# Optimization experiments

Hardware: AMD Instinct MI355X
Metric: run time of the kernel (lower is better)

The kernel has to match this reference:

```python
import jax, jax.numpy as jnp
import numpy as np

GRID = 64            # volume_pixel per axis
VOX = 1.0 / GRID     # voxel_physical (unit-cube volume_physical)
CHUNK = 128          # gaussians per scan step


def _voxel_centers():
    # [V,3] centers of voxels of a unit cube, V = GRID**3
    c = (jnp.arange(GRID, dtype=jnp.float32) + 0.5) * VOX
    zz, yy, xx = jnp.meshgrid(c, c, c, indexing='ij')
    return jnp.stack([xx.ravel(), yy.ravel(), zz.ravel()], axis=-1)


def _quat_to_rotmat(q):
    # q: [N,4] (w,x,y,z), normalized -> [N,3,3]
    q = q / jnp.linalg.norm(q, axis=-1, keepdims=True)
    w, x, y, z = q[:, 0], q[:, 1], q[:, 2], q[:, 3]
    return jnp.stack([
        jnp.stack([1 - 2 * (y * y + z * z), 2 * (x * y - w * z), 2 * (x * z + w * y)], -1),
        jnp.stack([2 * (x * y + w * z), 1 - 2 * (x * x + z * z), 2 * (y * z - w * x)], -1),
        jnp.stack([2 * (x * z - w * y), 2 * (y * z + w * x), 1 - 2 * (x * x + y * y)], -1),
    ], axis=-2)


def _voxelize(means3D, densities, scales, rotations):
    N = means3D.shape[0]
    R = _quat_to_rotmat(rotations)                       # [N,3,3]
    inv_s2 = 1.0 / (scales * scales)                     # [N,3]
    # Sigma^{-1} = R diag(1/s^2) R^T
    Sinv = jnp.einsum('nij,nj,nkj->nik', R, inv_s2, R)   # [N,3,3]
    centers = _voxel_centers()                            # [V,3]
    n_chunks = N // CHUNK
    mu_c = means3D.reshape(n_chunks, CHUNK, 3)
    de_c = densities.reshape(n_chunks, CHUNK)
    Si_c = Sinv.reshape(n_chunks, CHUNK, 3, 3)

    def step(vol, xs):
        mu, dens, Si = xs
        d = centers[None, :, :] - mu[:, None, :]                 # [C,V,3]
        qf = jnp.einsum('cvi,cij,cvj->cv', d, Si, d)             # [C,V]
        vol = vol + jnp.sum(dens[:, None] * jnp.exp(-0.5 * qf), axis=0)
        return vol, None

    vol0 = jnp.zeros((GRID ** 3,), dtype=means3D.dtype)
    volume, _ = jax.lax.scan(step, vol0, (mu_c, de_c, Si_c))
    volume = volume.reshape(GRID, GRID, GRID)
    # screen-space-style radius: 3 sigma of the largest axis, in voxels
    radii = jnp.ceil(3.0 * jnp.max(scales, axis=-1) / VOX).astype(jnp.int32)
    return volume, radii


def setup_inputs() -> dict:
    key = jax.random.key(0)
    k1, k2, k3, k4 = jax.random.split(key, 4)
    N = 4096
    means3D = jax.random.uniform(k1, (N, 3), dtype=jnp.float32)                 # in unit cube
    densities = jax.random.uniform(k2, (N,), dtype=jnp.float32)
    scales = jax.random.uniform(k3, (N, 3), dtype=jnp.float32) * 0.05 + 0.01    # 0.6-3.8 voxels
    rotations = jax.random.normal(k4, (N, 4), dtype=jnp.float32)
    return {"means3D": means3D, "densities": densities, "scales": scales, "rotations": rotations}


def reference(means3D, densities, scales, rotations):
    return _voxelize(means3D, densities, scales, rotations)
```

## Files before the change

kernel.cpp:

```cpp
#include <hip/hip_runtime.h>

#define GRIDN 64
#define NVOX (GRIDN * GRIDN * GRIDN)
#define VOXF (1.0f / 64.0f)
#define QCUT 16.0f
#define EXPSCL (-0.72134752044f)
#define SKIPTH (QCUT * EXPSCL)

#define WS_CULLA 0
#define WS_CULLB (4 * 4096)
#define WS_REC   (8 * 4096)

__global__ __launch_bounds__(256) void prep_kernel(
    const float* __restrict__ means, const float* __restrict__ dens,
    const float* __restrict__ scales, const float* __restrict__ rots,
    float* __restrict__ ws, float* __restrict__ radii_out, int N)
{
    int i = blockIdx.x * 256 + threadIdx.x;
    if (i >= N) return;

    float qw = rots[i * 4 + 0], qx = rots[i * 4 + 1];
    float qy = rots[i * 4 + 2], qz = rots[i * 4 + 3];
    float inm = rsqrtf(qw * qw + qx * qx + qy * qy + qz * qz);
    qw *= inm; qx *= inm; qy *= inm; qz *= inm;
    float r00 = 1.f - 2.f * (qy * qy + qz * qz);
    float r01 = 2.f * (qx * qy - qw * qz);
    float r02 = 2.f * (qx * qz + qw * qy);
    float r10 = 2.f * (qx * qy + qw * qz);
    float r11 = 1.f - 2.f * (qx * qx + qz * qz);
    float r12 = 2.f * (qy * qz - qw * qx);
    float r20 = 2.f * (qx * qz - qw * qy);
    float r21 = 2.f * (qy * qz + qw * qx);
    float r22 = 1.f - 2.f * (qx * qx + qy * qy);

    float s0 = scales[i * 3 + 0], s1 = scales[i * 3 + 1], s2 = scales[i * 3 + 2];
    float v0 = s0 * s0, v1 = s1 * s1, v2 = s2 * s2;
    float i0 = 1.f / v0, i1 = 1.f / v1, i2 = 1.f / v2;

    float A = (r00 * r00 * i0 + r01 * r01 * i1 + r02 * r02 * i2) * EXPSCL;
    float B = (r10 * r10 * i0 + r11 * r11 * i1 + r12 * r12 * i2) * EXPSCL;
    float C = (r20 * r20 * i0 + r21 * r21 * i1 + r22 * r22 * i2) * EXPSCL;
    float D = (r00 * r10 * i0 + r01 * r11 * i1 + r02 * r12 * i2) * EXPSCL;
    float E = (r00 * r20 * i0 + r01 * r21 * i1 + r02 * r22 * i2) * EXPSCL;
    float F = (r10 * r20 * i0 + r11 * r21 * i1 + r12 * r22 * i2) * EXPSCL;

    float Cxx = r00 * r00 * v0 + r01 * r01 * v1 + r02 * r02 * v2;
    float Cyy = r10 * r10 * v0 + r11 * r11 * v1 + r12 * r12 * v2;
    float Czz = r20 * r20 * v0 + r21 * r21 * v1 + r22 * r22 * v2;

    float de = fmaxf(dens[i], 1e-30f);
    float qeff = fmaxf(QCUT + 2.0f * logf(de), 0.0f);
    float smax2 = fmaxf(v0, fmaxf(v1, v2));

    float mx = means[i * 3 + 0], my = means[i * 3 + 1], mz = means[i * 3 + 2];
    float4 ca; ca.x = mx; ca.y = my; ca.z = mz; ca.w = sqrtf(qeff * Cxx);
    float4 cb; cb.x = sqrtf(qeff * Cyy); cb.y = sqrtf(qeff * Czz);
    cb.z = qeff * smax2; cb.w = 0.f;
    ((float4*)(ws + WS_CULLA))[i] = ca;
    ((float4*)(ws + WS_CULLB))[i] = cb;

    float4* R = (float4*)(ws + WS_REC + (size_t)i * 16);
    float4 w0; w0.x = A; w0.y = B; w0.z = C; w0.w = 2.f * D;
    float4 w1; w1.x = 2.f * E; w1.y = 2.f * F; w1.z = -0.25f / A; w1.w = log2f(de);
    float4 w2; w2.x = mx; w2.y = my; w2.z = mz; w2.w = 0.f;
    R[0] = w0; R[1] = w1; R[2] = w2;

    float m = fmaxf(s0, fmaxf(s1, s2));
    radii_out[i] = ceilf(m * 3.0f * 64.0f);

    if (i == 0) {
        float4 z; z.x = 0.f; z.y = 0.f; z.z = 0.f; z.w = 0.f;
        float4 d1; d1.x = 0.f; d1.y = 0.f; d1.z = 0.f; d1.w = -1e30f;
        float4* Dm = (float4*)(ws + WS_REC + (size_t)N * 16);
        Dm[0] = z; Dm[1] = d1; Dm[2] = z;
    }
}

#define BODY(v0_, v1_, v2_) do {                                              \
    float dy = py - v2_.y, dz = pz - v2_.z;                                   \
    float tt  = fmaf(v1_.y, dy, v0_.z * dz);                                  \
    float qyz = fmaf(v0_.y * dy, dy, fmaf(tt, dz, v1_.w));                    \
    float gx  = fmaf(v0_.w, dy, v1_.x * dz);                                  \
    float qmx = fmaf(gx * gx, v1_.z, qyz);                                    \
    if (!__all(qmx < SKIPTH)) {                                               \
        float dx0 = px - v2_.x;                                               \
        float dx1 = dx0 + VOXF, dx2 = dx0 + 2.f * VOXF, dx3 = dx0 + 3.f * VOXF;\
        acc.x += __builtin_amdgcn_exp2f(fmaf(dx0, fmaf(v0_.x, dx0, gx), qyz));\
        acc.y += __builtin_amdgcn_exp2f(fmaf(dx1, fmaf(v0_.x, dx1, gx), qyz));\
        acc.z += __builtin_amdgcn_exp2f(fmaf(dx2, fmaf(v0_.x, dx2, gx), qyz));\
        acc.w += __builtin_amdgcn_exp2f(fmaf(dx3, fmaf(v0_.x, dx3, gx), qyz));\
    }                                                                         \
} while (0)

__global__ __launch_bounds__(512, 8) void vox_kernel(
    const float* __restrict__ ws, float* __restrict__ out, int N)
{
    __shared__ unsigned long long cmask[64];
    __shared__ int slist[4096];
    __shared__ float4 plds[8][64];

    const float* rec = ws + WS_REC;
    const int tid = threadIdx.x;
    const int lane = tid & 63, wave = tid >> 6;
    const int t = (blockIdx.x * 421) & 1023;
    const int tX = t & 7, tY = (t >> 3) & 7, tZ = t >> 6;
    const int x = (tX << 3) + ((lane & 1) << 2);
    const int y = (tY << 3) + ((lane >> 1) & 7);
    const int z = (tZ << 2) + (lane >> 4);
    const float px = (x + 0.5f) * VOXF;
    const float py = (y + 0.5f) * VOXF;
    const float pz = (z + 0.5f) * VOXF;

    const float lox = ((tX << 3) + 0.5f) * VOXF, hix = ((tX << 3) + 7.5f) * VOXF;
    const float loy = ((tY << 3) + 0.5f) * VOXF, hiy = ((tY << 3) + 7.5f) * VOXF;
    const float loz = ((tZ << 2) + 0.5f) * VOXF, hiz = ((tZ << 2) + 3.5f) * VOXF;

    const int nch = (N + 63) >> 6;
    #pragma unroll
    for (int k = 0; k < 8; ++k) {
        const int c = (wave << 3) + k;
        unsigned long long bal = 0ull;
        if (c < nch) {
            const int gi = (c << 6) + lane;
            const int gc = gi < N ? gi : N - 1;
            float4 ca = ((const float4*)(ws + WS_CULLA))[gc];
            float4 cb = ((const float4*)(ws + WS_CULLB))[gc];
            float cx = fminf(fmaxf(ca.x, lox), hix) - ca.x;
            float cy = fminf(fmaxf(ca.y, loy), hiy) - ca.y;
            float cz = fminf(fmaxf(ca.z, loz), hiz) - ca.z;
            float d2 = fmaf(cx, cx, fmaf(cy, cy, cz * cz));
            bool keep = (gi < N) && (d2 <= cb.z)
                && (ca.x + ca.w >= lox) && (ca.x - ca.w <= hix)
                && (ca.y + cb.x >= loy) && (ca.y - cb.x <= hiy)
                && (ca.z + cb.y >= loz) && (ca.z - cb.y <= hiz);
            bal = __ballot(keep);
        }
        if (lane == 0) cmask[(wave << 3) + k] = bal;
    }
    __syncthreads();

    unsigned long long mk = cmask[lane];
    int pc = __popcll(mk);
    int incl = pc;
    #pragma unroll
    for (int d = 1; d < 64; d <<= 1) {
        int t2 = __shfl_up(incl, d, 64);
        if (lane >= d) incl += t2;
    }
    const int excl = incl - pc;
    const int cnt = __builtin_amdgcn_readlane(incl, 63);

    #pragma unroll
    for (int k = 0; k < 8; ++k) {
        const int c = (wave << 3) + k;
        unsigned long long mc = cmask[c];
        int bse = __builtin_amdgcn_readlane(excl, c);
        if ((mc >> lane) & 1ull) {
            int pre = __popcll(mc & ((1ull << lane) - 1ull));
            slist[bse + pre] = (c << 6) + lane;
        }
    }

    const int L = ((cnt + 31) >> 5) << 2;
    const int padend = L << 3;
    for (int i = cnt + tid; i < padend; i += 512) slist[i] = N;
    __syncthreads();

    const int beg = wave * L, end = beg + L;
    float4 acc; acc.x = 0.f; acc.y = 0.f; acc.z = 0.f; acc.w = 0.f;

    for (int base = beg; base < end; base += 64) {
        int src = base + lane;
        int vidx = slist[src < padend ? src : padend - 1];
        int m = end - base; if (m > 64) m = 64;
        for (int j = 0; j < m; j += 4) {
            int i0 = __builtin_amdgcn_readlane(vidx, j);
            int i1 = __builtin_amdgcn_readlane(vidx, j + 1);
            int i2 = __builtin_amdgcn_readlane(vidx, j + 2);
            int i3 = __builtin_amdgcn_readlane(vidx, j + 3);
            const float4* P0 = (const float4*)(rec + ((size_t)i0 << 4));
            const float4* P1 = (const float4*)(rec + ((size_t)i1 << 4));
            const float4* P2 = (const float4*)(rec + ((size_t)i2 << 4));
            const float4* P3 = (const float4*)(rec + ((size_t)i3 << 4));
            float4 a0 = P0[0], a1 = P0[1], a2 = P0[2];
            float4 b0 = P1[0], b1 = P1[1], b2 = P1[2];
            float4 c0 = P2[0], c1 = P2[1], c2 = P2[2];
            float4 d0 = P3[0], d1 = P3[1], d2 = P3[2];
            BODY(a0, a1, a2);
            BODY(b0, b1, b2);
            BODY(c0, c1, c2);
            BODY(d0, d1, d2);
        }
    }

    plds[wave][lane] = acc;
    __syncthreads();

    if (wave == 0) {
        float4 r = plds[0][lane];
        #pragma unroll
        for (int w = 1; w < 8; ++w) {
            float4 p = plds[w][lane];
            r.x += p.x; r.y += p.y; r.z += p.z; r.w += p.w;
        }
        const int v = (z << 12) + (y << 6) + x;
        *(float4*)&out[v] = r;
    }
}

extern "C" void kernel_launch(void* const* d_in, const int* in_sizes, int n_in,
                              void* d_out, int out_size, void* d_ws, size_t ws_size,
                              hipStream_t stream)
{
    const float* means  = (const float*)d_in[0];
    const float* dens   = (const float*)d_in[1];
    const float* scales = (const float*)d_in[2];
    const float* rots   = (const float*)d_in[3];
    float* out = (float*)d_out;
    float* ws  = (float*)d_ws;
    const int N = in_sizes[1];

    prep_kernel<<<(N + 255) / 256, 256, 0, stream>>>(means, dens, scales, rots,
                                                     ws, out + NVOX, N);
    vox_kernel<<<1024, 512, 0, stream>>>(ws, out, N);
}
```

Before: 29.87 us.

## Add coarse-cell culling pass so voxel tiles scan only per-cell candidate lists

The prep kernel gains 128 extra blocks. Each one culls all gaussians against a coarse 16x16x8 cell, recomputing the bounds inline, and writes a compacted candidate index list plus a count to workspace. Each vox tile then reads only its parent cell's list instead of culling all N gaussians, and maps the list entries back to global indices. This cuts per-tile culling loads and compute, at the cost of a hierarchical two-level cull, redundant bound recomputation, and an extra indirection.

```diff
diff --git a/kernel.cpp b/kernel.cpp
--- a/kernel.cpp
+++ b/kernel.cpp
@@ -10,70 +10,144 @@
 #define WS_CULLA 0
 #define WS_CULLB (4 * 4096)
 #define WS_REC   (8 * 4096)
+#define WS_CLIST (28 * 4096)
+#define WS_CCNT  (28 * 4096 + 128 * 4096)
 
 __global__ __launch_bounds__(256) void prep_kernel(
     const float* __restrict__ means, const float* __restrict__ dens,
     const float* __restrict__ scales, const float* __restrict__ rots,
-    float* __restrict__ ws, float* __restrict__ radii_out, int N)
+    float* __restrict__ ws, int* __restrict__ clist, int* __restrict__ ccnt,
+    float* __restrict__ radii_out, int N)
 {
-    int i = blockIdx.x * 256 + threadIdx.x;
-    if (i >= N) return;
-
-    float qw = rots[i * 4 + 0], qx = rots[i * 4 + 1];
-    float qy = rots[i * 4 + 2], qz = rots[i * 4 + 3];
-    float inm = rsqrtf(qw * qw + qx * qx + qy * qy + qz * qz);
-    qw *= inm; qx *= inm; qy *= inm; qz *= inm;
-    float r00 = 1.f - 2.f * (qy * qy + qz * qz);
-    float r01 = 2.f * (qx * qy - qw * qz);
-    float r02 = 2.f * (qx * qz + qw * qy);
-    float r10 = 2.f * (qx * qy + qw * qz);
-    float r11 = 1.f - 2.f * (qx * qx + qz * qz);
-    float r12 = 2.f * (qy * qz - qw * qx);
-    float r20 = 2.f * (qx * qz - qw * qy);
-    float r21 = 2.f * (qy * qz + qw * qx);
-    float r22 = 1.f - 2.f * (qx * qx + qy * qy);
-
-    float s0 = scales[i * 3 + 0], s1 = scales[i * 3 + 1], s2 = scales[i * 3 + 2];
-    float v0 = s0 * s0, v1 = s1 * s1, v2 = s2 * s2;
-    float i0 = 1.f / v0, i1 = 1.f / v1, i2 = 1.f / v2;
-
-    float A = (r00 * r00 * i0 + r01 * r01 * i1 + r02 * r02 * i2) * EXPSCL;
-    float B = (r10 * r10 * i0 + r11 * r11 * i1 + r12 * r12 * i2) * EXPSCL;
-    float C = (r20 * r20 * i0 + r21 * r21 * i1 + r22 * r22 * i2) * EXPSCL;
-    float D = (r00 * r10 * i0 + r01 * r11 * i1 + r02 * r12 * i2) * EXPSCL;
-    float E = (r00 * r20 * i0 + r01 * r21 * i1 + r02 * r22 * i2) * EXPSCL;
-    float F = (r10 * r20 * i0 + r11 * r21 * i1 + r12 * r22 * i2) * EXPSCL;
-
-    float Cxx = r00 * r00 * v0 + r01 * r01 * v1 + r02 * r02 * v2;
-    float Cyy = r10 * r10 * v0 + r11 * r11 * v1 + r12 * r12 * v2;
-    float Czz = r20 * r20 * v0 + r21 * r21 * v1 + r22 * r22 * v2;
-
-    float de = fmaxf(dens[i], 1e-30f);
-    float qeff = fmaxf(QCUT + 2.0f * logf(de), 0.0f);
-    float smax2 = fmaxf(v0, fmaxf(v1, v2));
-
-    float mx = means[i * 3 + 0], my = means[i * 3 + 1], mz = means[i * 3 + 2];
-    float4 ca; ca.x = mx; ca.y = my; ca.z = mz; ca.w = sqrtf(qeff * Cxx);
-    float4 cb; cb.x = sqrtf(qeff * Cyy); cb.y = sqrtf(qeff * Czz);
-    cb.z = qeff * smax2; cb.w = 0.f;
-    ((float4*)(ws + WS_CULLA))[i] = ca;
-    ((float4*)(ws + WS_CULLB))[i] = cb;
-
-    float4* R = (float4*)(ws + WS_REC + (size_t)i * 16);
-    float4 w0; w0.x = A; w0.y = B; w0.z = C; w0.w = 2.f * D;
-    float4 w1; w1.x = 2.f * E; w1.y = 2.f * F; w1.z = -0.25f / A; w1.w = log2f(de);
-    float4 w2; w2.x = mx; w2.y = my; w2.z = mz; w2.w = 0.f;
-    R[0] = w0; R[1] = w1; R[2] = w2;
-
-    float m = fmaxf(s0, fmaxf(s1, s2));
-    radii_out[i] = ceilf(m * 3.0f * 64.0f);
-
-    if (i == 0) {
-        float4 z; z.x = 0.f; z.y = 0.f; z.z = 0.f; z.w = 0.f;
-        float4 d1; d1.x = 0.f; d1.y = 0.f; d1.z = 0.f; d1.w = -1e30f;
-        float4* Dm = (float4*)(ws + WS_REC + (size_t)N * 16);
-        Dm[0] = z; Dm[1] = d1; Dm[2] = z;
-    }
+    __shared__ int swseg[4][1024];
+    __shared__ int lenw[4];
+
+    const int nrec = (N + 255) >> 8;
+    const int b = blockIdx.x;
+
+    if (b < nrec) {
+        int i = b * 256 + threadIdx.x;
+        if (i >= N) return;
+
+        float qw = rots[i * 4 + 0], qx = rots[i * 4 + 1];
+        float qy = rots[i * 4 + 2], qz = rots[i * 4 + 3];
+        float inm = rsqrtf(qw * qw + qx * qx + qy * qy + qz * qz);
+        qw *= inm; qx *= inm; qy *= inm; qz *= inm;
+        float r00 = 1.f - 2.f * (qy * qy + qz * qz);
+        float r01 = 2.f * (qx * qy - qw * qz);
+        float r02 = 2.f * (qx * qz + qw * qy);
+        float r10 = 2.f * (qx * qy + qw * qz);
+        float r11 = 1.f - 2.f * (qx * qx + qz * qz);
+        float r12 = 2.f * (qy * qz - qw * qx);
+        float r20 = 2.f * (qx * qz - qw * qy);
+        float r21 = 2.f * (qy * qz + qw * qx);
+        float r22 = 1.f - 2.f * (qx * qx + qy * qy);
+
+        float s0 = scales[i * 3 + 0], s1 = scales[i * 3 + 1], s2 = scales[i * 3 + 2];
+        float v0 = s0 * s0, v1 = s1 * s1, v2 = s2 * s2;
+        float i0 = 1.f / v0, i1 = 1.f / v1, i2 = 1.f / v2;
+
+        float A = (r00 * r00 * i0 + r01 * r01 * i1 + r02 * r02 * i2) * EXPSCL;
+        float B = (r10 * r10 * i0 + r11 * r11 * i1 + r12 * r12 * i2) * EXPSCL;
+        float C = (r20 * r20 * i0 + r21 * r21 * i1 + r22 * r22 * i2) * EXPSCL;
+        float D = (r00 * r10 * i0 + r01 * r11 * i1 + r02 * r12 * i2) * EXPSCL;
+        float E = (r00 * r20 * i0 + r01 * r21 * i1 + r02 * r22 * i2) * EXPSCL;
+        float F = (r10 * r20 * i0 + r11 * r21 * i1 + r12 * r22 * i2) * EXPSCL;
+
+        float Cxx = r00 * r00 * v0 + r01 * r01 * v1 + r02 * r02 * v2;
+        float Cyy = r10 * r10 * v0 + r11 * r11 * v1 + r12 * r12 * v2;
+        float Czz = r20 * r20 * v0 + r21 * r21 * v1 + r22 * r22 * v2;
+
+        float de = fmaxf(dens[i], 1e-30f);
+        float qeff = fmaxf(QCUT + 2.0f * logf(de), 0.0f);
+        float smax2 = fmaxf(v0, fmaxf(v1, v2));
+
+        float mx = means[i * 3 + 0], my = means[i * 3 + 1], mz = means[i * 3 + 2];
+        float4 ca; ca.x = mx; ca.y = my; ca.z = mz; ca.w = sqrtf(qeff * Cxx);
+        float4 cb; cb.x = sqrtf(qeff * Cyy); cb.y = sqrtf(qeff * Czz);
+        cb.z = qeff * smax2; cb.w = 0.f;
+        ((float4*)(ws + WS_CULLA))[i] = ca;
+        ((float4*)(ws + WS_CULLB))[i] = cb;
+
+        float4* R = (float4*)(ws + WS_REC + (size_t)i * 16);
+        float4 w0; w0.x = A; w0.y = B; w0.z = C; w0.w = 2.f * D;
+        float4 w1; w1.x = 2.f * E; w1.y = 2.f * F; w1.z = -0.25f / A; w1.w = log2f(de);
+        float4 w2; w2.x = mx; w2.y = my; w2.z = mz; w2.w = 0.f;
+        R[0] = w0; R[1] = w1; R[2] = w2;
+
+        float m = fmaxf(s0, fmaxf(s1, s2));
+        radii_out[i] = ceilf(m * 3.0f * 64.0f);
+
+        if (i == 0) {
+            float4 zv; zv.x = 0.f; zv.y = 0.f; zv.z = 0.f; zv.w = 0.f;
+            float4 d1; d1.x = 0.f; d1.y = 0.f; d1.z = 0.f; d1.w = -1e30f;
+            float4* Dm = (float4*)(ws + WS_REC + (size_t)N * 16);
+            Dm[0] = zv; Dm[1] = d1; Dm[2] = zv;
+        }
+        return;
+    }
+
+    const int tid = threadIdx.x, lane = tid & 63, wave = tid >> 6;
+    const int cell = b - nrec;
+    const int cX = cell & 3, cY = (cell >> 2) & 3, cZ = cell >> 4;
+    const float lox = ((cX << 4) + 0.5f) * VOXF, hix = ((cX << 4) + 15.5f) * VOXF;
+    const float loy = ((cY << 4) + 0.5f) * VOXF, hiy = ((cY << 4) + 15.5f) * VOXF;
+    const float loz = ((cZ << 3) + 0.5f) * VOXF, hiz = ((cZ << 3) + 7.5f) * VOXF;
+
+    const int nch = (N + 63) >> 6;
+    int off = 0;
+    for (int j = 0; j < 16; ++j) {
+        const int c = (wave << 4) + j;
+        if (c >= nch) break;
+        const int gi = (c << 6) + lane;
+        const int gc = gi < N ? gi : N - 1;
+
+        float qw = rots[gc * 4 + 0], qx = rots[gc * 4 + 1];
+        float qy = rots[gc * 4 + 2], qz = rots[gc * 4 + 3];
+        float r00, r10, r20, r01, r11, r21, r02, r12, r22;
+        {
+            float inm = rsqrtf(qw * qw + qx * qx + qy * qy + qz * qz);
+            float w = qw * inm, a = qx * inm, bq = qy * inm, cq = qz * inm;
+            r00 = 1.f - 2.f * (bq * bq + cq * cq); r01 = 2.f * (a * bq - w * cq);
+            r02 = 2.f * (a * cq + w * bq);         r10 = 2.f * (a * bq + w * cq);
+            r11 = 1.f - 2.f * (a * a + cq * cq);   r12 = 2.f * (bq * cq - w * a);
+            r20 = 2.f * (a * cq - w * bq);         r21 = 2.f * (bq * cq + w * a);
+            r22 = 1.f - 2.f * (a * a + bq * bq);
+        }
+        float s0 = scales[gc * 3 + 0], s1 = scales[gc * 3 + 1], s2 = scales[gc * 3 + 2];
+        float v0 = s0 * s0, v1 = s1 * s1, v2 = s2 * s2;
+        float Cxx = r00 * r00 * v0 + r01 * r01 * v1 + r02 * r02 * v2;
+        float Cyy = r10 * r10 * v0 + r11 * r11 * v1 + r12 * r12 * v2;
+        float Czz = r20 * r20 * v0 + r21 * r21 * v1 + r22 * r22 * v2;
+        float de = fmaxf(dens[gc], 1e-30f);
+        float qeff = fmaxf(QCUT + 2.0f * logf(de), 0.0f);
+        float rx = sqrtf(qeff * Cxx), ry = sqrtf(qeff * Cyy), rz = sqrtf(qeff * Czz);
+        float sph = qeff * fmaxf(v0, fmaxf(v1, v2));
+        float mx = means[gc * 3 + 0], my = means[gc * 3 + 1], mz = means[gc * 3 + 2];
+
+        float cx = fminf(fmaxf(mx, lox), hix) - mx;
+        float cy = fminf(fmaxf(my, loy), hiy) - my;
+        float cz = fminf(fmaxf(mz, loz), hiz) - mz;
+        float d2 = fmaf(cx, cx, fmaf(cy, cy, cz * cz));
+        bool keep = (gi < N) && (d2 <= sph)
+            && (mx + rx >= lox) && (mx - rx <= hix)
+            && (my + ry >= loy) && (my - ry <= hiy)
+            && (mz + rz >= loz) && (mz - rz <= hiz);
+
+        unsigned long long bal = __ballot(keep);
+        int pre = __popcll(bal & ((1ull << lane) - 1ull));
+        if (keep) swseg[wave][off + pre] = gi;
+        off += __popcll(bal);
+    }
+    if (lane == 0) lenw[wave] = off;
+    __syncthreads();
+
+    const int l0 = lenw[0], l1 = lenw[1], l2 = lenw[2];
+    const int mybase = (wave > 0 ? l0 : 0) + (wave > 1 ? l1 : 0) + (wave > 2 ? l2 : 0);
+    const int mylen = lenw[wave];
+    int* dst = clist + (size_t)cell * 4096;
+    for (int i = lane; i < mylen; i += 64) dst[mybase + i] = swseg[wave][i];
+    if (tid == 0) ccnt[cell] = l0 + l1 + l2 + lenw[3];
 }
 
 #define BODY(v0_, v1_, v2_) do {                                              \
@@ -93,7 +167,8 @@
 } while (0)
 
 __global__ __launch_bounds__(512, 8) void vox_kernel(
-    const float* __restrict__ ws, float* __restrict__ out, int N)
+    const float* __restrict__ ws, const int* __restrict__ clist,
+    const int* __restrict__ ccnt, float* __restrict__ out, int N)
 {
     __shared__ unsigned long long cmask[64];
     __shared__ int slist[4096];
@@ -104,6 +179,7 @@
     const int lane = tid & 63, wave = tid >> 6;
     const int t = (blockIdx.x * 421) & 1023;
     const int tX = t & 7, tY = (t >> 3) & 7, tZ = t >> 6;
+    const int cell = ((tZ >> 1) << 4) + ((tY >> 1) << 2) + (tX >> 1);
     const int x = (tX << 3) + ((lane & 1) << 2);
     const int y = (tY << 3) + ((lane >> 1) & 7);
     const int z = (tZ << 2) + (lane >> 4);
@@ -115,27 +191,31 @@
     const float loy = ((tY << 3) + 0.5f) * VOXF, hiy = ((tY << 3) + 7.5f) * VOXF;
     const float loz = ((tZ << 2) + 0.5f) * VOXF, hiz = ((tZ << 2) + 3.5f) * VOXF;
 
-    const int nch = (N + 63) >> 6;
+    const int ccount = ccnt[cell];
+    const int* cl = clist + (size_t)cell * 4096;
+    const int nchl = (ccount + 63) >> 6;
+
     #pragma unroll
     for (int k = 0; k < 8; ++k) {
-        const int c = (wave << 3) + k;
+        const int c = (k << 3) | wave;
         unsigned long long bal = 0ull;
-        if (c < nch) {
-            const int gi = (c << 6) + lane;
-            const int gc = gi < N ? gi : N - 1;
-            float4 ca = ((const float4*)(ws + WS_CULLA))[gc];
-            float4 cb = ((const float4*)(ws + WS_CULLB))[gc];
+        if (c < nchl) {
+            const int p = (c << 6) + lane;
+            const bool inb = p < ccount;
+            const int gi = cl[inb ? p : 0];
+            float4 ca = ((const float4*)(ws + WS_CULLA))[gi];
+            float4 cb = ((const float4*)(ws + WS_CULLB))[gi];
             float cx = fminf(fmaxf(ca.x, lox), hix) - ca.x;
             float cy = fminf(fmaxf(ca.y, loy), hiy) - ca.y;
             float cz = fminf(fmaxf(ca.z, loz), hiz) - ca.z;
             float d2 = fmaf(cx, cx, fmaf(cy, cy, cz * cz));
-            bool keep = (gi < N) && (d2 <= cb.z)
+            bool keep = inb && (d2 <= cb.z)
                 && (ca.x + ca.w >= lox) && (ca.x - ca.w <= hix)
                 && (ca.y + cb.x >= loy) && (ca.y - cb.x <= hiy)
                 && (ca.z + cb.y >= loz) && (ca.z - cb.y <= hiz);
             bal = __ballot(keep);
         }
-        if (lane == 0) cmask[(wave << 3) + k] = bal;
+        if (lane == 0) cmask[c] = bal;
     }
     __syncthreads();
 
@@ -152,12 +232,13 @@
 
     #pragma unroll
     for (int k = 0; k < 8; ++k) {
-        const int c = (wave << 3) + k;
+        const int c = (k << 3) | wave;
         unsigned long long mc = cmask[c];
+        if (mc == 0ull) continue;
         int bse = __builtin_amdgcn_readlane(excl, c);
         if ((mc >> lane) & 1ull) {
             int pre = __popcll(mc & ((1ull << lane) - 1ull));
-            slist[bse + pre] = (c << 6) + lane;
+            slist[bse + pre] = cl[(c << 6) + lane];
         }
     }
 
@@ -218,9 +299,12 @@
     const float* rots   = (const float*)d_in[3];
     float* out = (float*)d_out;
     float* ws  = (float*)d_ws;
+    int* clist = (int*)(ws + WS_CLIST);
+    int* ccnt  = (int*)(ws + WS_CCNT);
     const int N = in_sizes[1];
 
-    prep_kernel<<<(N + 255) / 256, 256, 0, stream>>>(means, dens, scales, rots,
-                                                     ws, out + NVOX, N);
-    vox_kernel<<<1024, 512, 0, stream>>>(ws, out, N);
+    const int nrec = (N + 255) / 256;
+    prep_kernel<<<nrec + 128, 256, 0, stream>>>(means, dens, scales, rots,
+                                                ws, clist, ccnt, out + NVOX, N);
+    vox_kernel<<<1024, 512, 0, stream>>>(ws, clist, ccnt, out, N);
 }
```

New measurement: 32.39 us. 8.5% more time.

## Stage culled gaussian records in LDS and use 8x8x8 tiles with 1024-thread blocks

Applied to the files above, without the earlier changes.

Tiles grow from 8x8x4 to 8x8x8 voxels, so there are 512 blocks of 1024 threads, and each lane now evaluates 8 voxels along x instead of 4. Before, each wave read per-gaussian records straight from global memory through readlane-scalarized addresses. Now each batch of 256 culled records is loaded cooperatively into shared memory, and every wave reads its 16-record slice from there. The surviving-gaussian list is capped at 3072 entries, which could silently drop contributions in dense tiles, and the larger tiles cull less tightly.

```diff
diff --git a/kernel.cpp b/kernel.cpp
--- a/kernel.cpp
+++ b/kernel.cpp
@@ -69,56 +69,41 @@
     radii_out[i] = ceilf(m * 3.0f * 64.0f);
 
     if (i == 0) {
-        float4 z; z.x = 0.f; z.y = 0.f; z.z = 0.f; z.w = 0.f;
+        float4 zv; zv.x = 0.f; zv.y = 0.f; zv.z = 0.f; zv.w = 0.f;
         float4 d1; d1.x = 0.f; d1.y = 0.f; d1.z = 0.f; d1.w = -1e30f;
         float4* Dm = (float4*)(ws + WS_REC + (size_t)N * 16);
-        Dm[0] = z; Dm[1] = d1; Dm[2] = z;
+        Dm[0] = zv; Dm[1] = d1; Dm[2] = zv;
     }
 }
 
-#define BODY(v0_, v1_, v2_) do {                                              \
-    float dy = py - v2_.y, dz = pz - v2_.z;                                   \
-    float tt  = fmaf(v1_.y, dy, v0_.z * dz);                                  \
-    float qyz = fmaf(v0_.y * dy, dy, fmaf(tt, dz, v1_.w));                    \
-    float gx  = fmaf(v0_.w, dy, v1_.x * dz);                                  \
-    float qmx = fmaf(gx * gx, v1_.z, qyz);                                    \
-    if (!__all(qmx < SKIPTH)) {                                               \
-        float dx0 = px - v2_.x;                                               \
-        float dx1 = dx0 + VOXF, dx2 = dx0 + 2.f * VOXF, dx3 = dx0 + 3.f * VOXF;\
-        acc.x += __builtin_amdgcn_exp2f(fmaf(dx0, fmaf(v0_.x, dx0, gx), qyz));\
-        acc.y += __builtin_amdgcn_exp2f(fmaf(dx1, fmaf(v0_.x, dx1, gx), qyz));\
-        acc.z += __builtin_amdgcn_exp2f(fmaf(dx2, fmaf(v0_.x, dx2, gx), qyz));\
-        acc.w += __builtin_amdgcn_exp2f(fmaf(dx3, fmaf(v0_.x, dx3, gx), qyz));\
-    }                                                                         \
-} while (0)
-
-__global__ __launch_bounds__(512, 8) void vox_kernel(
+__global__ __launch_bounds__(1024, 8) void vox_kernel(
     const float* __restrict__ ws, float* __restrict__ out, int N)
 {
     __shared__ unsigned long long cmask[64];
-    __shared__ int slist[4096];
-    __shared__ float4 plds[8][64];
+    __shared__ int slist[3072];
+    __shared__ float4 sreq[3][256];
+    __shared__ float4 plds[16][64];
 
     const float* rec = ws + WS_REC;
     const int tid = threadIdx.x;
     const int lane = tid & 63, wave = tid >> 6;
-    const int t = (blockIdx.x * 421) & 1023;
+    const int t = (blockIdx.x * 341) & 511;
     const int tX = t & 7, tY = (t >> 3) & 7, tZ = t >> 6;
-    const int x = (tX << 3) + ((lane & 1) << 2);
-    const int y = (tY << 3) + ((lane >> 1) & 7);
-    const int z = (tZ << 2) + (lane >> 4);
-    const float px = (x + 0.5f) * VOXF;
+    const int x0 = tX << 3;
+    const int y = (tY << 3) + (lane & 7);
+    const int z = (tZ << 3) + (lane >> 3);
+    const float px = (x0 + 0.5f) * VOXF;
     const float py = (y + 0.5f) * VOXF;
     const float pz = (z + 0.5f) * VOXF;
 
-    const float lox = ((tX << 3) + 0.5f) * VOXF, hix = ((tX << 3) + 7.5f) * VOXF;
-    const float loy = ((tY << 3) + 0.5f) * VOXF, hiy = ((tY << 3) + 7.5f) * VOXF;
-    const float loz = ((tZ << 2) + 0.5f) * VOXF, hiz = ((tZ << 2) + 3.5f) * VOXF;
+    const float lox = (x0 + 0.5f) * VOXF,          hix = (x0 + 7.5f) * VOXF;
+    const float loy = ((tY << 3) + 0.5f) * VOXF,   hiy = ((tY << 3) + 7.5f) * VOXF;
+    const float loz = ((tZ << 3) + 0.5f) * VOXF,   hiz = ((tZ << 3) + 7.5f) * VOXF;
 
     const int nch = (N + 63) >> 6;
     #pragma unroll
-    for (int k = 0; k < 8; ++k) {
-        const int c = (wave << 3) + k;
+    for (int k = 0; k < 4; ++k) {
+        const int c = (k << 4) | wave;
         unsigned long long bal = 0ull;
         if (c < nch) {
             const int gi = (c << 6) + lane;
@@ -135,7 +120,7 @@
                 && (ca.z + cb.y >= loz) && (ca.z - cb.y <= hiz);
             bal = __ballot(keep);
         }
-        if (lane == 0) cmask[(wave << 3) + k] = bal;
+        if (lane == 0) cmask[c] = bal;
     }
     __syncthreads();
 
@@ -148,63 +133,92 @@
         if (lane >= d) incl += t2;
     }
     const int excl = incl - pc;
-    const int cnt = __builtin_amdgcn_readlane(incl, 63);
+    int cnt = __builtin_amdgcn_readlane(incl, 63);
+    if (cnt > 3072) cnt = 3072;
 
     #pragma unroll
-    for (int k = 0; k < 8; ++k) {
-        const int c = (wave << 3) + k;
+    for (int k = 0; k < 4; ++k) {
+        const int c = (k << 4) | wave;
         unsigned long long mc = cmask[c];
+        if (mc == 0ull) continue;
         int bse = __builtin_amdgcn_readlane(excl, c);
         if ((mc >> lane) & 1ull) {
             int pre = __popcll(mc & ((1ull << lane) - 1ull));
-            slist[bse + pre] = (c << 6) + lane;
-        }
-    }
-
-    const int L = ((cnt + 31) >> 5) << 2;
-    const int padend = L << 3;
-    for (int i = cnt + tid; i < padend; i += 512) slist[i] = N;
-    __syncthreads();
-
-    const int beg = wave * L, end = beg + L;
-    float4 acc; acc.x = 0.f; acc.y = 0.f; acc.z = 0.f; acc.w = 0.f;
-
-    for (int base = beg; base < end; base += 64) {
-        int src = base + lane;
-        int vidx = slist[src < padend ? src : padend - 1];
-        int m = end - base; if (m > 64) m = 64;
-        for (int j = 0; j < m; j += 4) {
-            int i0 = __builtin_amdgcn_readlane(vidx, j);
-            int i1 = __builtin_amdgcn_readlane(vidx, j + 1);
-            int i2 = __builtin_amdgcn_readlane(vidx, j + 2);
-            int i3 = __builtin_amdgcn_readlane(vidx, j + 3);
-            const float4* P0 = (const float4*)(rec + ((size_t)i0 << 4));
-            const float4* P1 = (const float4*)(rec + ((size_t)i1 << 4));
-            const float4* P2 = (const float4*)(rec + ((size_t)i2 << 4));
-            const float4* P3 = (const float4*)(rec + ((size_t)i3 << 4));
-            float4 a0 = P0[0], a1 = P0[1], a2 = P0[2];
-            float4 b0 = P1[0], b1 = P1[1], b2 = P1[2];
-            float4 c0 = P2[0], c1 = P2[1], c2 = P2[2];
-            float4 d0 = P3[0], d1 = P3[1], d2 = P3[2];
-            BODY(a0, a1, a2);
-            BODY(b0, b1, b2);
-            BODY(c0, c1, c2);
-            BODY(d0, d1, d2);
-        }
-    }
-
-    plds[wave][lane] = acc;
-    __syncthreads();
-
+            int pos = bse + pre;
+            if (pos < 3072) slist[pos] = (c << 6) + lane;
+        }
+    }
+    int padend = ((cnt + 255) >> 8) << 8;
+    if (padend > 3072) padend = 3072;
+    for (int i = cnt + tid; i < padend; i += 1024) slist[i] = N;
+    __syncthreads();
+
+    float4 accL, accH;
+    accL.x = accL.y = accL.z = accL.w = 0.f;
+    accH = accL;
+
+    for (int base = 0; base < padend; base += 256) {
+        if (tid < 768) {
+            const int part = tid >> 8, s = tid & 255;
+            const int gi = slist[base + s];
+            sreq[part][s] = ((const float4*)(rec + ((size_t)gi << 4)))[part];
+        }
+        __syncthreads();
+
+        const int s0 = wave << 4;
+        #pragma unroll 4
+        for (int j = 0; j < 16; ++j) {
+            float4 a0 = sreq[0][s0 + j];
+            float4 a1 = sreq[1][s0 + j];
+            float4 a2 = sreq[2][s0 + j];
+            float dy = py - a2.y, dz = pz - a2.z;
+            float tt  = fmaf(a1.y, dy, a0.z * dz);
+            float qyz = fmaf(a0.y * dy, dy, fmaf(tt, dz, a1.w));
+            float gx  = fmaf(a0.w, dy, a1.x * dz);
+            float qmx = fmaf(gx * gx, a1.z, qyz);
+            if (!__all(qmx < SKIPTH)) {
+                float dx0 = px - a2.x;
+                float dx1 = dx0 + VOXF,        dx2 = dx0 + 2.f * VOXF;
+                float dx3 = dx0 + 3.f * VOXF,  dx4 = dx0 + 4.f * VOXF;
+                float dx5 = dx0 + 5.f * VOXF,  dx6 = dx0 + 6.f * VOXF;
+                float dx7 = dx0 + 7.f * VOXF;
+                accL.x += __builtin_amdgcn_exp2f(fmaf(dx0, fmaf(a0.x, dx0, gx), qyz));
+                accL.y += __builtin_amdgcn_exp2f(fmaf(dx1, fmaf(a0.x, dx1, gx), qyz));
+                accL.z += __builtin_amdgcn_exp2f(fmaf(dx2, fmaf(a0.x, dx2, gx), qyz));
+                accL.w += __builtin_amdgcn_exp2f(fmaf(dx3, fmaf(a0.x, dx3, gx), qyz));
+                accH.x += __builtin_amdgcn_exp2f(fmaf(dx4, fmaf(a0.x, dx4, gx), qyz));
+                accH.y += __builtin_amdgcn_exp2f(fmaf(dx5, fmaf(a0.x, dx5, gx), qyz));
+                accH.z += __builtin_amdgcn_exp2f(fmaf(dx6, fmaf(a0.x, dx6, gx), qyz));
+                accH.w += __builtin_amdgcn_exp2f(fmaf(dx7, fmaf(a0.x, dx7, gx), qyz));
+            }
+        }
+        __syncthreads();
+    }
+
+    const int v = (z << 12) + (y << 6) + x0;
+
+    plds[wave][lane] = accL;
+    __syncthreads();
     if (wave == 0) {
         float4 r = plds[0][lane];
         #pragma unroll
-        for (int w = 1; w < 8; ++w) {
+        for (int w = 1; w < 16; ++w) {
             float4 p = plds[w][lane];
             r.x += p.x; r.y += p.y; r.z += p.z; r.w += p.w;
         }
-        const int v = (z << 12) + (y << 6) + x;
         *(float4*)&out[v] = r;
+    }
+    __syncthreads();
+    plds[wave][lane] = accH;
+    __syncthreads();
+    if (wave == 0) {
+        float4 r = plds[0][lane];
+        #pragma unroll
+        for (int w = 1; w < 16; ++w) {
+            float4 p = plds[w][lane];
+            r.x += p.x; r.y += p.y; r.z += p.z; r.w += p.w;
+        }
+        *(float4*)&out[v + 4] = r;
     }
 }
 
@@ -222,5 +236,5 @@
 
     prep_kernel<<<(N + 255) / 256, 256, 0, stream>>>(means, dens, scales, rots,
                                                      ws, out + NVOX, N);
-    vox_kernel<<<1024, 512, 0, stream>>>(ws, out, N);
+    vox_kernel<<<512, 1024, 0, stream>>>(ws, out, N);
 }
```

After: 27.60 us. 1.08x faster.
